# Kernel optimization log

Hardware: AMD Instinct MI355X
Metric: run time of the kernel (lower is better)

The kernel has to match this reference:

```python
import jax, jax.numpy as jnp
import numpy as np

B, N, C, H = 2, 2048, 768, 12
D = C // H  # head dim = 64


def _rotate_half(x):
    d2 = x.shape[-1] // 2
    x1, x2 = x[..., :d2], x[..., d2:]
    return jnp.concatenate([-x2, x1], axis=-1)


def _apply_rope(x, sin, cos):
    # x: [B,H,N,D], sin/cos: [N,D] -> broadcast over (B,H)
    return x * cos[None, None] + _rotate_half(x) * sin[None, None]


def setup_inputs() -> dict:
    key = jax.random.key(0)
    ks = jax.random.split(key, 7)
    x = jax.random.normal(ks[0], (B, N, C), dtype=jnp.float32)
    sin_spatial = jax.random.normal(ks[1], (N, D), dtype=jnp.float32)
    cos_spatial = jax.random.normal(ks[2], (N, D), dtype=jnp.float32)
    s = 1.0 / np.sqrt(C)
    W_qkv = jax.random.uniform(ks[3], (C, 3 * C), jnp.float32, -s, s)
    b_qkv = jax.random.uniform(ks[4], (3 * C,), jnp.float32, -s, s)
    W_out = jax.random.uniform(ks[5], (C, C), jnp.float32, -s, s)
    b_out = jax.random.uniform(ks[6], (C,), jnp.float32, -s, s)
    return {"x": x, "sin_spatial": sin_spatial, "cos_spatial": cos_spatial,
            "W_qkv": W_qkv, "b_qkv": b_qkv, "W_out": W_out, "b_out": b_out}


def reference(x, sin_spatial, cos_spatial, W_qkv, b_qkv, W_out, b_out):
    qkv = x @ W_qkv + b_qkv                       # [B,N,3C]
    qkv = qkv.reshape(B, N, 3, H, D).transpose(2, 0, 3, 1, 4)  # [3,B,H,N,D]
    q, k, v = qkv[0], qkv[1], qkv[2]
    q = _apply_rope(q, sin_spatial, cos_spatial)
    k = _apply_rope(k, sin_spatial, cos_spatial)
    att = jnp.einsum('bhqd,bhkd->bhqk', q, k) * (D ** -0.5)
    att = jax.nn.softmax(att, axis=-1)            # dropout is identity (eval)
    y = jnp.einsum('bhqk,bhkd->bhqd', att, v)     # [B,H,N,D]
    y = y.transpose(0, 2, 1, 3).reshape(B, N, C)
    return y @ W_out + b_out
```

## Files before the change

### kernel.cpp

```cpp
#include <hip/hip_runtime.h>
#include <hip/hip_bf16.h>

#define BB 2
#define NN 2048
#define CC 768
#define HH 12
#define DD 64
#define MM 4096
#define N3 2304

typedef __attribute__((ext_vector_type(8))) short bf16x8;
typedef __attribute__((ext_vector_type(4))) float f32x4;

#define QSCALE 0.18033688011112043f


__device__ __forceinline__ unsigned short f2bf(float f) {
    union { float f; unsigned u; } v; v.f = f;
    unsigned r = v.u + 0x7FFFu + ((v.u >> 16) & 1u);
    return (unsigned short)(r >> 16);
}

__device__ __forceinline__ short f2bf_rn(float f) {
    union { __hip_bfloat16 h; short s; } v;
    v.h = __float2bfloat16(f);
    return v.s;
}

__device__ __forceinline__ float exp2_hw(float x) {
    float r;
    asm("v_exp_f32 %0, %1" : "=v"(r) : "v"(x));
    return r;
}

__device__ __forceinline__ bf16x8 ld_frag(const unsigned short* p) {
    bf16x8 r;
    __builtin_memcpy(&r, p, 8);
    __builtin_memcpy((char*)&r + 8, p + 16, 8);
    return r;
}

__device__ __forceinline__ bf16x8 ld_frag16(const unsigned short* p) {
    bf16x8 r;
    __builtin_memcpy(&r, p, 16);
    return r;
}

__global__ void k_cvt(const float* __restrict__ s, unsigned short* __restrict__ d, int n4) {
    int i = blockIdx.x * blockDim.x + threadIdx.x;
    int st = gridDim.x * blockDim.x;
    for (; i < n4; i += st) {
        float4 v = ((const float4*)s)[i];
        ushort4 o;
        o.x = f2bf(v.x); o.y = f2bf(v.y); o.z = f2bf(v.z); o.w = f2bf(v.w);
        ((ushort4*)d)[i] = o;
    }
}

__global__ void k_cvtT(const float* __restrict__ s, unsigned short* __restrict__ d,
                       int R, int Cc) {
    __shared__ unsigned short t[64][72];
    const int c0 = blockIdx.x * 64, r0 = blockIdx.y * 64;
    const int tr = threadIdx.x >> 4;
    const int tc = (threadIdx.x & 15) * 4;
#pragma unroll
    for (int i = 0; i < 4; i++) {
        int r = tr + i * 16;
        float4 v = *(const float4*)(s + (size_t)(r0 + r) * Cc + c0 + tc);
        t[tc + 0][r] = f2bf(v.x);
        t[tc + 1][r] = f2bf(v.y);
        t[tc + 2][r] = f2bf(v.z);
        t[tc + 3][r] = f2bf(v.w);
    }
    __syncthreads();
    const int wr = threadIdx.x >> 2;
    const int wc = (threadIdx.x & 3) * 16;
    *(uint4*)(d + (size_t)(c0 + wr) * R + r0 + wc)     = *(uint4*)&t[wr][wc];
    *(uint4*)(d + (size_t)(c0 + wr) * R + r0 + wc + 8) = *(uint4*)&t[wr][wc + 8];
}

__launch_bounds__(256)
__global__ void k_qkv(const unsigned short* __restrict__ xb,
                      const unsigned short* __restrict__ wt,
                      const float* __restrict__ bias,
                      const float* __restrict__ sinp,
                      const float* __restrict__ cosp,
                      unsigned short* __restrict__ qws,
                      unsigned short* __restrict__ kws,
                      unsigned short* __restrict__ vws) {
    __shared__ unsigned short As[128][40];
    __shared__ unsigned short Bs[64][40];
    const int tid = threadIdx.x;
    const int lane = tid & 63, w = tid >> 6;
    const int ql = lane & 15, lg = lane >> 4;
    const int row0 = blockIdx.x * 128;
    const int j0 = blockIdx.y * 64;

    f32x4 acc[2][4];
#pragma unroll
    for (int a = 0; a < 2; a++)
#pragma unroll
        for (int b = 0; b < 4; b++) acc[a][b] = f32x4{0.f, 0.f, 0.f, 0.f};

    const int ar = tid >> 1, ac = (tid & 1) * 16;
    const int jr = tid >> 2, kc = (tid & 3) * 8;

    for (int k0 = 0; k0 < CC; k0 += 32) {
        uint4 av0 = *(const uint4*)(xb + (size_t)(row0 + ar) * CC + k0 + ac);
        uint4 av1 = *(const uint4*)(xb + (size_t)(row0 + ar) * CC + k0 + ac + 8);
        uint4 bv  = *(const uint4*)(wt + (size_t)(j0 + jr) * CC + k0 + kc);
        *(uint4*)&As[ar][ac]     = av0;
        *(uint4*)&As[ar][ac + 8] = av1;
        *(uint4*)&Bs[jr][kc]     = bv;
        __syncthreads();

        bf16x8 af[2], bfr[4];
#pragma unroll
        for (int fr = 0; fr < 2; fr++) af[fr] = ld_frag(&As[w * 32 + fr * 16 + ql][lg * 4]);
#pragma unroll
        for (int fn = 0; fn < 4; fn++) bfr[fn] = ld_frag(&Bs[fn * 16 + ql][lg * 4]);
#pragma unroll
        for (int fr = 0; fr < 2; fr++)
#pragma unroll
            for (int fn = 0; fn < 4; fn++)
                acc[fr][fn] = __builtin_amdgcn_mfma_f32_16x16x32_bf16(af[fr], bfr[fn], acc[fr][fn], 0, 0, 0);
        __syncthreads();
    }

    float vals[2][4][4];
#pragma unroll
    for (int fr = 0; fr < 2; fr++)
#pragma unroll
        for (int fn = 0; fn < 4; fn++) {
            float bj = bias[j0 + fn * 16 + ql];
#pragma unroll
            for (int r = 0; r < 4; r++) vals[fr][fn][r] = acc[fr][fn][r] + bj;
        }
    const int t = j0 / CC;
    const int h = (j0 % CC) >> 6;
    if (t < 2) {
        unsigned short* outp = (t == 0) ? qws : kws;
        const float qs = (t == 0) ? QSCALE : 1.0f;
#pragma unroll
        for (int fr = 0; fr < 2; fr++)
#pragma unroll
            for (int r = 0; r < 4; r++) {
                int m = row0 + w * 32 + fr * 16 + lg * 4 + r;
                int b = m >> 11, n = m & (NN - 1);
#pragma unroll
                for (int fn = 0; fn < 4; fn++) {
                    int d = fn * 16 + ql;
                    float cv = cosp[n * DD + d], sv = sinp[n * DD + d];
                    float other = vals[fr][fn ^ 2][r];
                    float rv = (vals[fr][fn][r] * cv + ((fn < 2) ? -other : other) * sv) * qs;
                    int dcol = (t == 0) ? d
                             : ((fn >> 1) * 32 + (ql >> 2) * 8 + (fn & 1) * 4 + (ql & 3));
                    outp[((size_t)(b * HH + h) * NN + n) * DD + dcol] = f2bf(rv);
                }
            }
    } else {
#pragma unroll
        for (int fr = 0; fr < 2; fr++)
#pragma unroll
            for (int r = 0; r < 4; r++) {
                int m = row0 + w * 32 + fr * 16 + lg * 4 + r;
                int b = m >> 11, n = m & (NN - 1);
                int ncol = (n & ~31) + lg * 8 + (fr & 1) * 4 + r;
#pragma unroll
                for (int fn = 0; fn < 4; fn++) {
                    int d = fn * 16 + ql;
                    vws[((size_t)(b * HH + h) * DD + d) * NN + ncol] = f2bf(vals[fr][fn][r]);
                }
            }
    }
}

__launch_bounds__(128)
__global__ void k_attn(const unsigned short* __restrict__ qws,
                       const unsigned short* __restrict__ kws,
                       const unsigned short* __restrict__ vws,
                       unsigned short* __restrict__ yws) {
    __shared__ unsigned short Ks[2][64][72];
    __shared__ unsigned short Vs[2][64][72];
    const int tid = threadIdx.x;
    const int lane = tid & 63, w = tid >> 6;
    const int ql = lane & 15, lg = lane >> 4;
    const int d0 = blockIdx.x;
    const int bh = (d0 & 7) + 8 * (d0 >> 8);
    const int qb = (d0 >> 3) & 31;
    const int qw = qb * 64 + w * 32;
    const unsigned short* Qp = qws + (size_t)bh * NN * DD;
    const unsigned short* Kp = kws + (size_t)bh * NN * DD;
    const unsigned short* Vp = vws + (size_t)bh * DD * NN;

    bf16x8 qf[2][2];
#pragma unroll
    for (int fn = 0; fn < 2; fn++)
#pragma unroll
        for (int kb = 0; kb < 2; kb++)
            qf[fn][kb] = ld_frag(Qp + (size_t)(qw + fn * 16 + ql) * DD + kb * 32 + lg * 4);

    f32x4 oacc[4][2];
#pragma unroll
    for (int a = 0; a < 4; a++)
#pragma unroll
        for (int b = 0; b < 2; b++) oacc[a][b] = f32x4{0.f, 0.f, 0.f, 0.f};
    float mrun[2] = {-1e30f, -1e30f}, lrun[2] = {0.f, 0.f};

    const int srow = tid >> 1;
    const int shalf = (tid & 1) * 32;

#pragma unroll
    for (int j = 0; j < 4; j++) {
        *(uint4*)&Ks[0][srow][shalf + j * 8] = *(const uint4*)(Kp + (size_t)srow * DD + shalf + j * 8);
        *(uint4*)&Vs[0][srow][shalf + j * 8] = *(const uint4*)(Vp + (size_t)srow * NN + shalf + j * 8);
    }
    __syncthreads();

    const int NT = NN / 64;
    int cur = 0;
    for (int kt = 0; kt < NT; kt++) {
        uint4 kn[4], vn[4];
        const bool hasn = (kt + 1 < NT);
        if (hasn) {
#pragma unroll
            for (int j = 0; j < 4; j++) {
                kn[j] = *(const uint4*)(Kp + (size_t)((kt + 1) * 64 + srow) * DD + shalf + j * 8);
                vn[j] = *(const uint4*)(Vp + (size_t)srow * NN + (kt + 1) * 64 + shalf + j * 8);
            }
        }
        const unsigned short (*Kc)[72] = Ks[cur];
        const unsigned short (*Vc)[72] = Vs[cur];

        f32x4 sacc[4][2];
#pragma unroll
        for (int a = 0; a < 4; a++)
#pragma unroll
            for (int b = 0; b < 2; b++) sacc[a][b] = f32x4{0.f, 0.f, 0.f, 0.f};
        __builtin_amdgcn_s_setprio(1);
#pragma unroll
        for (int kb = 0; kb < 2; kb++) {
            bf16x8 kf[4];
#pragma unroll
            for (int fr = 0; fr < 4; fr++)
                kf[fr] = ld_frag16(&Kc[fr * 16 + ql][kb * 32 + lg * 8]);
#pragma unroll
            for (int fr = 0; fr < 4; fr++)
#pragma unroll
                for (int fn = 0; fn < 2; fn++)
                    sacc[fr][fn] = __builtin_amdgcn_mfma_f32_16x16x32_bf16(kf[fr], qf[fn][kb], sacc[fr][fn], 0, 0, 0);
        }
        __builtin_amdgcn_s_setprio(0);

        bf16x8 pB[2][2];
#pragma unroll
        for (int fn = 0; fn < 2; fn++) {
            float ma = fmaxf(fmaxf(sacc[0][fn][0], sacc[0][fn][1]), fmaxf(sacc[0][fn][2], sacc[0][fn][3]));
            float mb = fmaxf(fmaxf(sacc[1][fn][0], sacc[1][fn][1]), fmaxf(sacc[1][fn][2], sacc[1][fn][3]));
            float mc = fmaxf(fmaxf(sacc[2][fn][0], sacc[2][fn][1]), fmaxf(sacc[2][fn][2], sacc[2][fn][3]));
            float md = fmaxf(fmaxf(sacc[3][fn][0], sacc[3][fn][1]), fmaxf(sacc[3][fn][2], sacc[3][fn][3]));
            float tm = fmaxf(fmaxf(ma, mb), fmaxf(mc, md));
            tm = fmaxf(tm, __shfl_xor(tm, 16));
            tm = fmaxf(tm, __shfl_xor(tm, 32));
            if (__any(tm > mrun[fn] + 8.0f)) {
                float mn = fmaxf(mrun[fn], tm);
                float scl = exp2_hw(mrun[fn] - mn);
                lrun[fn] *= scl;
#pragma unroll
                for (int db = 0; db < 4; db++) oacc[db][fn] *= scl;
                mrun[fn] = mn;
            }
            float ts = 0.f;
#pragma unroll
            for (int fr = 0; fr < 4; fr++)
#pragma unroll
                for (int r = 0; r < 4; r++) {
                    float p = exp2_hw(sacc[fr][fn][r] - mrun[fn]);
                    sacc[fr][fn][r] = p;
                    ts += p;
                }
            ts += __shfl_xor(ts, 16);
            ts += __shfl_xor(ts, 32);
            lrun[fn] += ts;

#pragma unroll
            for (int kkb = 0; kkb < 2; kkb++) {
                bf16x8 t8;
#pragma unroll
                for (int e = 0; e < 8; e++)
                    t8[e] = f2bf_rn(sacc[kkb * 2 + (e >> 2)][fn][e & 3]);
                pB[fn][kkb] = t8;
            }
        }

        __builtin_amdgcn_s_setprio(1);
#pragma unroll
        for (int db = 0; db < 4; db++) {
            bf16x8 va[2];
#pragma unroll
            for (int kkb = 0; kkb < 2; kkb++)
                va[kkb] = ld_frag16(&Vc[db * 16 + ql][kkb * 32 + lg * 8]);
#pragma unroll
            for (int kkb = 0; kkb < 2; kkb++)
#pragma unroll
                for (int fn = 0; fn < 2; fn++)
                    oacc[db][fn] = __builtin_amdgcn_mfma_f32_16x16x32_bf16(va[kkb], pB[fn][kkb], oacc[db][fn], 0, 0, 0);
        }
        __builtin_amdgcn_s_setprio(0);

        if (hasn) {
#pragma unroll
            for (int j = 0; j < 4; j++) {
                *(uint4*)&Ks[cur ^ 1][srow][shalf + j * 8] = kn[j];
                *(uint4*)&Vs[cur ^ 1][srow][shalf + j * 8] = vn[j];
            }
            __syncthreads();
            cur ^= 1;
        }
    }

    const int b = bh / HH, h = bh % HH;
#pragma unroll
    for (int fn = 0; fn < 2; fn++) {
        float inv = 1.0f / lrun[fn];
        int q = qw + fn * 16 + ql;
        unsigned short* yp = yws + (size_t)(b * NN + q) * CC + h * DD + lg * 4;
#pragma unroll
        for (int db = 0; db < 4; db++) {
            ushort4 o;
            o.x = f2bf(oacc[db][fn][0] * inv);
            o.y = f2bf(oacc[db][fn][1] * inv);
            o.z = f2bf(oacc[db][fn][2] * inv);
            o.w = f2bf(oacc[db][fn][3] * inv);
            *(ushort4*)(yp + db * 16) = o;
        }
    }
}

__launch_bounds__(256)
__global__ void k_out(const unsigned short* __restrict__ yb,
                      const unsigned short* __restrict__ wt,
                      const float* __restrict__ bias,
                      float* __restrict__ out) {
    __shared__ unsigned short As[128][40];
    __shared__ unsigned short Bs[64][40];
    const int tid = threadIdx.x;
    const int lane = tid & 63, w = tid >> 6;
    const int ql = lane & 15, lg = lane >> 4;
    const int row0 = blockIdx.x * 128;
    const int j0 = blockIdx.y * 64;

    f32x4 acc[2][4];
#pragma unroll
    for (int a = 0; a < 2; a++)
#pragma unroll
        for (int b = 0; b < 4; b++) acc[a][b] = f32x4{0.f, 0.f, 0.f, 0.f};

    const int ar = tid >> 1, ac = (tid & 1) * 16;
    const int jr = tid >> 2, kc = (tid & 3) * 8;

    for (int k0 = 0; k0 < CC; k0 += 32) {
        uint4 av0 = *(const uint4*)(yb + (size_t)(row0 + ar) * CC + k0 + ac);
        uint4 av1 = *(const uint4*)(yb + (size_t)(row0 + ar) * CC + k0 + ac + 8);
        uint4 bv  = *(const uint4*)(wt + (size_t)(j0 + jr) * CC + k0 + kc);
        *(uint4*)&As[ar][ac]     = av0;
        *(uint4*)&As[ar][ac + 8] = av1;
        *(uint4*)&Bs[jr][kc]     = bv;
        __syncthreads();

        bf16x8 af[2], bfr[4];
#pragma unroll
        for (int fr = 0; fr < 2; fr++) af[fr] = ld_frag(&As[w * 32 + fr * 16 + ql][lg * 4]);
#pragma unroll
        for (int fn = 0; fn < 4; fn++) bfr[fn] = ld_frag(&Bs[fn * 16 + ql][lg * 4]);
#pragma unroll
        for (int fr = 0; fr < 2; fr++)
#pragma unroll
            for (int fn = 0; fn < 4; fn++)
                acc[fr][fn] = __builtin_amdgcn_mfma_f32_16x16x32_bf16(af[fr], bfr[fn], acc[fr][fn], 0, 0, 0);
        __syncthreads();
    }

#pragma unroll
    for (int fr = 0; fr < 2; fr++)
#pragma unroll
        for (int fn = 0; fn < 4; fn++) {
            float bj = bias[j0 + fn * 16 + ql];
#pragma unroll
            for (int r = 0; r < 4; r++) {
                int m = row0 + w * 32 + fr * 16 + lg * 4 + r;
                out[(size_t)m * CC + j0 + fn * 16 + ql] = acc[fr][fn][r] + bj;
            }
        }
}

extern "C" void kernel_launch(void* const* d_in, const int* in_sizes, int n_in,
                              void* d_out, int out_size, void* d_ws, size_t ws_size,
                              hipStream_t stream) {
    const float* x    = (const float*)d_in[0];
    const float* sinp = (const float*)d_in[1];
    const float* cosp = (const float*)d_in[2];
    const float* wqkv = (const float*)d_in[3];
    const float* bqkv = (const float*)d_in[4];
    const float* wout = (const float*)d_in[5];
    const float* bout = (const float*)d_in[6];
    float* out = (float*)d_out;
    char* ws = (char*)d_ws;

    unsigned short* xb  = (unsigned short*)(ws);
    unsigned short* wqb = (unsigned short*)(ws + 6291456);
    unsigned short* wob = (unsigned short*)(ws + 9830400);
    unsigned short* qws = (unsigned short*)(ws + 11010048);
    unsigned short* kws = (unsigned short*)(ws + 17301504);
    unsigned short* vws = (unsigned short*)(ws + 23592960);
    unsigned short* yws = (unsigned short*)(ws + 29884416);
    if (ws_size < 36175872) return;

    k_cvt<<<dim3(512), dim3(256), 0, stream>>>(x, xb, MM * CC / 4);
    k_cvtT<<<dim3(36, 12), dim3(256), 0, stream>>>(wqkv, wqb, CC, N3);
    k_cvtT<<<dim3(12, 12), dim3(256), 0, stream>>>(wout, wob, CC, CC);
    k_qkv<<<dim3(32, 36), dim3(256), 0, stream>>>(xb, wqb, bqkv, sinp, cosp, qws, kws, vws);
    k_attn<<<dim3(768), dim3(128), 0, stream>>>(qws, kws, vws, yws);
    k_out<<<dim3(32, 12), dim3(256), 0, stream>>>(yws, wob, bout, out);
}
```

Baseline: 136.3 us.

## Software-pipeline QK^T one tile ahead of softmax/PV with a triple-buffered V tile

After: 180.9 us. 32.8% more time.

```diff
diff --git a/kernel.cpp b/kernel.cpp
--- a/kernel.cpp
+++ b/kernel.cpp
@@ -153,8 +153,7 @@
                     float cv = cosp[n * DD + d], sv = sinp[n * DD + d];
                     float other = vals[fr][fn ^ 2][r];
                     float rv = (vals[fr][fn][r] * cv + ((fn < 2) ? -other : other) * sv) * qs;
-                    int dcol = (t == 0) ? d
-                             : ((fn >> 1) * 32 + (ql >> 2) * 8 + (fn & 1) * 4 + (ql & 3));
+                    int dcol = (fn >> 1) * 32 + (ql >> 2) * 8 + (fn & 1) * 4 + (ql & 3);
                     outp[((size_t)(b * HH + h) * NN + n) * DD + dcol] = f2bf(rv);
                 }
             }
@@ -181,7 +180,7 @@
                        const unsigned short* __restrict__ vws,
                        unsigned short* __restrict__ yws) {
     __shared__ unsigned short Ks[2][64][72];
-    __shared__ unsigned short Vs[2][64][72];
+    __shared__ unsigned short Vs[3][64][72];
     const int tid = threadIdx.x;
     const int lane = tid & 63, w = tid >> 6;
     const int ql = lane & 15, lg = lane >> 4;
@@ -198,7 +197,7 @@
     for (int fn = 0; fn < 2; fn++)
 #pragma unroll
         for (int kb = 0; kb < 2; kb++)
-            qf[fn][kb] = ld_frag(Qp + (size_t)(qw + fn * 16 + ql) * DD + kb * 32 + lg * 4);
+            qf[fn][kb] = ld_frag16(Qp + (size_t)(qw + fn * 16 + ql) * DD + kb * 32 + lg * 8);
 
     f32x4 oacc[4][2];
 #pragma unroll
@@ -217,48 +216,83 @@
     }
     __syncthreads();
 
+    f32x4 sc[4][2];
+#pragma unroll
+    for (int a = 0; a < 4; a++)
+#pragma unroll
+        for (int b = 0; b < 2; b++) sc[a][b] = f32x4{0.f, 0.f, 0.f, 0.f};
+#pragma unroll
+    for (int kb = 0; kb < 2; kb++) {
+        bf16x8 kf[4];
+#pragma unroll
+        for (int fr = 0; fr < 4; fr++)
+            kf[fr] = ld_frag16(&Ks[0][fr * 16 + ql][kb * 32 + lg * 8]);
+#pragma unroll
+        for (int fr = 0; fr < 4; fr++)
+#pragma unroll
+            for (int fn = 0; fn < 2; fn++)
+                sc[fr][fn] = __builtin_amdgcn_mfma_f32_16x16x32_bf16(kf[fr], qf[fn][kb], sc[fr][fn], 0, 0, 0);
+    }
+
+    {
+        uint4 kn[4], vn[4];
+#pragma unroll
+        for (int j = 0; j < 4; j++) {
+            kn[j] = *(const uint4*)(Kp + (size_t)(64 + srow) * DD + shalf + j * 8);
+            vn[j] = *(const uint4*)(Vp + (size_t)srow * NN + 64 + shalf + j * 8);
+        }
+#pragma unroll
+        for (int j = 0; j < 4; j++) {
+            *(uint4*)&Ks[1][srow][shalf + j * 8] = kn[j];
+            *(uint4*)&Vs[1][srow][shalf + j * 8] = vn[j];
+        }
+    }
+    __syncthreads();
+
     const int NT = NN / 64;
-    int cur = 0;
-    for (int kt = 0; kt < NT; kt++) {
+    int vcur = 0;
+    for (int t = 0; t < NT; t++) {
+        const bool hasn1 = (t + 1 < NT);
+        const bool hasn2 = (t + 2 < NT);
         uint4 kn[4], vn[4];
-        const bool hasn = (kt + 1 < NT);
-        if (hasn) {
+        if (hasn2) {
 #pragma unroll
             for (int j = 0; j < 4; j++) {
-                kn[j] = *(const uint4*)(Kp + (size_t)((kt + 1) * 64 + srow) * DD + shalf + j * 8);
-                vn[j] = *(const uint4*)(Vp + (size_t)srow * NN + (kt + 1) * 64 + shalf + j * 8);
-            }
-        }
-        const unsigned short (*Kc)[72] = Ks[cur];
-        const unsigned short (*Vc)[72] = Vs[cur];
-
-        f32x4 sacc[4][2];
+                kn[j] = *(const uint4*)(Kp + (size_t)((t + 2) * 64 + srow) * DD + shalf + j * 8);
+                vn[j] = *(const uint4*)(Vp + (size_t)srow * NN + (t + 2) * 64 + shalf + j * 8);
+            }
+        }
+
+        f32x4 sn[4][2];
 #pragma unroll
         for (int a = 0; a < 4; a++)
 #pragma unroll
-            for (int b = 0; b < 2; b++) sacc[a][b] = f32x4{0.f, 0.f, 0.f, 0.f};
-        __builtin_amdgcn_s_setprio(1);
-#pragma unroll
-        for (int kb = 0; kb < 2; kb++) {
-            bf16x8 kf[4];
-#pragma unroll
-            for (int fr = 0; fr < 4; fr++)
-                kf[fr] = ld_frag16(&Kc[fr * 16 + ql][kb * 32 + lg * 8]);
-#pragma unroll
-            for (int fr = 0; fr < 4; fr++)
-#pragma unroll
-                for (int fn = 0; fn < 2; fn++)
-                    sacc[fr][fn] = __builtin_amdgcn_mfma_f32_16x16x32_bf16(kf[fr], qf[fn][kb], sacc[fr][fn], 0, 0, 0);
-        }
-        __builtin_amdgcn_s_setprio(0);
+            for (int b = 0; b < 2; b++) sn[a][b] = f32x4{0.f, 0.f, 0.f, 0.f};
+        if (hasn1) {
+            const unsigned short (*Kc)[72] = Ks[(t + 1) & 1];
+            __builtin_amdgcn_s_setprio(1);
+#pragma unroll
+            for (int kb = 0; kb < 2; kb++) {
+                bf16x8 kf[4];
+#pragma unroll
+                for (int fr = 0; fr < 4; fr++)
+                    kf[fr] = ld_frag16(&Kc[fr * 16 + ql][kb * 32 + lg * 8]);
+#pragma unroll
+                for (int fr = 0; fr < 4; fr++)
+#pragma unroll
+                    for (int fn = 0; fn < 2; fn++)
+                        sn[fr][fn] = __builtin_amdgcn_mfma_f32_16x16x32_bf16(kf[fr], qf[fn][kb], sn[fr][fn], 0, 0, 0);
+            }
+            __builtin_amdgcn_s_setprio(0);
+        }
 
         bf16x8 pB[2][2];
 #pragma unroll
         for (int fn = 0; fn < 2; fn++) {
-            float ma = fmaxf(fmaxf(sacc[0][fn][0], sacc[0][fn][1]), fmaxf(sacc[0][fn][2], sacc[0][fn][3]));
-            float mb = fmaxf(fmaxf(sacc[1][fn][0], sacc[1][fn][1]), fmaxf(sacc[1][fn][2], sacc[1][fn][3]));
-            float mc = fmaxf(fmaxf(sacc[2][fn][0], sacc[2][fn][1]), fmaxf(sacc[2][fn][2], sacc[2][fn][3]));
-            float md = fmaxf(fmaxf(sacc[3][fn][0], sacc[3][fn][1]), fmaxf(sacc[3][fn][2], sacc[3][fn][3]));
+            float ma = fmaxf(fmaxf(sc[0][fn][0], sc[0][fn][1]), fmaxf(sc[0][fn][2], sc[0][fn][3]));
+            float mb = fmaxf(fmaxf(sc[1][fn][0], sc[1][fn][1]), fmaxf(sc[1][fn][2], sc[1][fn][3]));
+            float mc = fmaxf(fmaxf(sc[2][fn][0], sc[2][fn][1]), fmaxf(sc[2][fn][2], sc[2][fn][3]));
+            float md = fmaxf(fmaxf(sc[3][fn][0], sc[3][fn][1]), fmaxf(sc[3][fn][2], sc[3][fn][3]));
             float tm = fmaxf(fmaxf(ma, mb), fmaxf(mc, md));
             tm = fmaxf(tm, __shfl_xor(tm, 16));
             tm = fmaxf(tm, __shfl_xor(tm, 32));
@@ -275,8 +309,8 @@
             for (int fr = 0; fr < 4; fr++)
 #pragma unroll
                 for (int r = 0; r < 4; r++) {
-                    float p = exp2_hw(sacc[fr][fn][r] - mrun[fn]);
-                    sacc[fr][fn][r] = p;
+                    float p = exp2_hw(sc[fr][fn][r] - mrun[fn]);
+                    sc[fr][fn][r] = p;
                     ts += p;
                 }
             ts += __shfl_xor(ts, 16);
@@ -288,35 +322,45 @@
                 bf16x8 t8;
 #pragma unroll
                 for (int e = 0; e < 8; e++)
-                    t8[e] = f2bf_rn(sacc[kkb * 2 + (e >> 2)][fn][e & 3]);
+                    t8[e] = f2bf_rn(sc[kkb * 2 + (e >> 2)][fn][e & 3]);
                 pB[fn][kkb] = t8;
             }
         }
 
-        __builtin_amdgcn_s_setprio(1);
-#pragma unroll
-        for (int db = 0; db < 4; db++) {
-            bf16x8 va[2];
-#pragma unroll
-            for (int kkb = 0; kkb < 2; kkb++)
-                va[kkb] = ld_frag16(&Vc[db * 16 + ql][kkb * 32 + lg * 8]);
-#pragma unroll
-            for (int kkb = 0; kkb < 2; kkb++)
-#pragma unroll
-                for (int fn = 0; fn < 2; fn++)
-                    oacc[db][fn] = __builtin_amdgcn_mfma_f32_16x16x32_bf16(va[kkb], pB[fn][kkb], oacc[db][fn], 0, 0, 0);
-        }
-        __builtin_amdgcn_s_setprio(0);
-
-        if (hasn) {
+        {
+            const unsigned short (*Vc)[72] = Vs[vcur];
+            __builtin_amdgcn_s_setprio(1);
+#pragma unroll
+            for (int db = 0; db < 4; db++) {
+                bf16x8 va[2];
+#pragma unroll
+                for (int kkb = 0; kkb < 2; kkb++)
+                    va[kkb] = ld_frag16(&Vc[db * 16 + ql][kkb * 32 + lg * 8]);
+#pragma unroll
+                for (int kkb = 0; kkb < 2; kkb++)
+#pragma unroll
+                    for (int fn = 0; fn < 2; fn++)
+                        oacc[db][fn] = __builtin_amdgcn_mfma_f32_16x16x32_bf16(va[kkb], pB[fn][kkb], oacc[db][fn], 0, 0, 0);
+            }
+            __builtin_amdgcn_s_setprio(0);
+        }
+
+        if (hasn2) {
+            int vw = vcur + 2; if (vw >= 3) vw -= 3;
 #pragma unroll
             for (int j = 0; j < 4; j++) {
-                *(uint4*)&Ks[cur ^ 1][srow][shalf + j * 8] = kn[j];
-                *(uint4*)&Vs[cur ^ 1][srow][shalf + j * 8] = vn[j];
-            }
+                *(uint4*)&Ks[t & 1][srow][shalf + j * 8] = kn[j];
+                *(uint4*)&Vs[vw][srow][shalf + j * 8] = vn[j];
+            }
+        }
+        if (hasn1) {
             __syncthreads();
-            cur ^= 1;
-        }
+#pragma unroll
+            for (int a = 0; a < 4; a++)
+#pragma unroll
+                for (int b = 0; b < 2; b++) sc[a][b] = sn[a][b];
+        }
+        vcur++; if (vcur >= 3) vcur -= 3;
     }
 
     const int b = bh / HH, h = bh % HH;
```
